# Performance work log

Hardware: AMD Instinct MI355X
Metric: run time of the kernel (lower is better)

Reference implementation:

```python
import jax, jax.numpy as jnp
import numpy as np

N_NODES = 50000
N_EDGES = 800000
NUM_GRAPHS = 512
IN_DIM = 128
HID = 128
OUT_DIM = 1


def setup_inputs() -> dict:
    key = jax.random.key(0)
    ks = jax.random.split(key, 8)
    x = jax.random.normal(ks[0], (N_NODES, IN_DIM), dtype=jnp.float32)
    edge_index = jax.random.randint(ks[1], (2, N_EDGES), 0, N_NODES, dtype=jnp.int64)
    batch = jnp.sort(jax.random.randint(ks[2], (N_NODES,), 0, NUM_GRAPHS, dtype=jnp.int64))
    s1 = 1.0 / np.sqrt(IN_DIM)
    s2 = 1.0 / np.sqrt(HID)
    W1 = jax.random.normal(ks[3], (IN_DIM, HID), dtype=jnp.float32) * s1
    b1 = jnp.zeros((HID,), dtype=jnp.float32)
    W2 = jax.random.normal(ks[4], (HID, HID), dtype=jnp.float32) * s2
    b2 = jnp.zeros((HID,), dtype=jnp.float32)
    Wl = jax.random.normal(ks[5], (HID, OUT_DIM), dtype=jnp.float32) * s2
    bl = jnp.zeros((OUT_DIM,), dtype=jnp.float32)
    return {"x": x, "edge_index": edge_index, "batch": batch,
            "W1": W1, "b1": b1, "W2": W2, "b2": b2, "Wl": Wl, "bl": bl}


def _gcn_conv(x, src, dst, norm, W, b):
    # GCNConv: D^{-1/2}(A+I)D^{-1/2} X W + b (self-loops already in src/dst)
    h = x @ W                                    # [N, H]
    msg = h[src] * norm[:, None]                 # gather + edge-normalize
    agg = jax.ops.segment_sum(msg, dst, num_segments=N_NODES)  # scatter-add
    return agg + b


def reference(x, edge_index, batch, W1, b1, W2, b2, Wl, bl):
    loops = jnp.arange(N_NODES, dtype=edge_index.dtype)
    src = jnp.concatenate([edge_index[0], loops])
    dst = jnp.concatenate([edge_index[1], loops])
    deg = jax.ops.segment_sum(jnp.ones_like(dst, dtype=x.dtype), dst, num_segments=N_NODES)
    dinv = jax.lax.rsqrt(deg)                    # deg >= 1 due to self-loops
    norm = dinv[src] * dinv[dst]                 # symmetric normalization per edge

    h = jax.nn.relu(_gcn_conv(x, src, dst, norm, W1, b1))
    h = jax.nn.relu(_gcn_conv(h, src, dst, norm, W2, b2))

    # global_mean_pool over graph ids
    sums = jax.ops.segment_sum(h, batch, num_segments=NUM_GRAPHS)
    cnts = jax.ops.segment_sum(jnp.ones((N_NODES,), dtype=h.dtype), batch, num_segments=NUM_GRAPHS)
    pooled = sums / jnp.maximum(cnts, 1.0)[:, None]

    out = jax.nn.sigmoid(pooled @ Wl + bl)       # [G, 1]
    return out.squeeze(1)                        # [G]
```

## Files before the change

kernel.cpp:

```cpp
#include <hip/hip_runtime.h>
#include <hip/hip_bf16.h>

#define N_NODES 50000
#define N_EDGES 800000
#define NUM_GRAPHS 512
#define MAXDEG 64
#define EPB 4096
#define P1_BLOCKS 196
#define NBUCK 256
#define NPB 196

typedef short short8 __attribute__((ext_vector_type(8)));
typedef unsigned short u16x8 __attribute__((ext_vector_type(8)));
typedef float f32x4 __attribute__((ext_vector_type(4)));

__device__ __forceinline__ unsigned short f2bu(float f) {
    __hip_bfloat16 h = __float2bfloat16(f);
    return *reinterpret_cast<unsigned short*>(&h);
}
__device__ __forceinline__ float bu2f(unsigned short u) {
    unsigned int v = ((unsigned int)u) << 16;
    float f;
    __builtin_memcpy(&f, &v, 4);
    return f;
}

__global__ __launch_bounds__(256) void bin_k(const int* __restrict__ ei,
                                             unsigned int* __restrict__ staging,
                                             int* __restrict__ cnts_tbl,
                                             int* __restrict__ offs_tbl,
                                             unsigned short* __restrict__ hs1,
                                             unsigned short* __restrict__ h1) {
    __shared__ unsigned int st[EPB];
    __shared__ int cnt[NBUCK], cur[NBUCK], scan[NBUCK];
    int b = blockIdx.x, t = threadIdx.x;
    if (b == 0 && t < 64)
        ((unsigned int*)(hs1 + (size_t)N_NODES * 128))[t] = 0u;
    if (b == 1 && t < 64)
        ((unsigned int*)(h1 + (size_t)N_NODES * 128))[t] = 0u;
    cnt[t] = 0;
    __syncthreads();

    int e0 = b * EPB;
    int srcv[16], dstv[16], bk[16];
#pragma unroll
    for (int k = 0; k < 16; ++k) {
        int e = e0 + k * 256 + t;
        bool ok = e < N_EDGES;
        srcv[k] = ok ? ei[e] : 0;
        dstv[k] = ok ? ei[N_EDGES + e] : 0;
        bk[k] = ok ? (dstv[k] / NPB) : -1;
        if (ok) atomicAdd(&cnt[bk[k]], 1);
    }
    __syncthreads();
    scan[t] = cnt[t];
    __syncthreads();
    for (int off = 1; off < 256; off <<= 1) {
        int u = t >= off ? scan[t - off] : 0;
        __syncthreads();
        scan[t] += u;
        __syncthreads();
    }
    int excl = scan[t] - cnt[t];
    cur[t] = excl;
    cnts_tbl[t * P1_BLOCKS + b] = cnt[t];
    offs_tbl[t * P1_BLOCKS + b] = excl;
    __syncthreads();
#pragma unroll
    for (int k = 0; k < 16; ++k) {
        if (bk[k] >= 0) {
            int pos = atomicAdd(&cur[bk[k]], 1);
            int dl = dstv[k] - bk[k] * NPB;
            st[pos] = (unsigned int)srcv[k] | ((unsigned int)dl << 16);
        }
    }
    __syncthreads();
    unsigned int* gout = staging + (size_t)b * EPB;
    for (int i = t; i < EPB; i += 256) gout[i] = st[i];
}

__global__ __launch_bounds__(256) void adjbuild_k(const unsigned int* __restrict__ staging,
                                                  const int* __restrict__ cnts_tbl,
                                                  const int* __restrict__ offs_tbl,
                                                  unsigned short* __restrict__ adj,
                                                  int* __restrict__ cnt,
                                                  float* __restrict__ dinv,
                                                  const float* __restrict__ W1,
                                                  const float* __restrict__ W2,
                                                  unsigned short* __restrict__ W1t,
                                                  unsigned short* __restrict__ W2t) {
    int b = blockIdx.x, t = threadIdx.x;
    if (b >= NBUCK) {
        int wb = b - NBUCK;
        const float* W = wb < 64 ? W1 : W2;
        unsigned short* Wt = wb < 64 ? W1t : W2t;
        int idx = (wb & 63) * 256 + t;
        int k = idx >> 7, n = idx & 127;
        Wt[n * 128 + k] = f2bu(W[idx]);
        return;
    }
    __shared__ unsigned short adjL[NPB * MAXDEG];
    __shared__ int cntL[NPB];
    __shared__ int segStart[P1_BLOCKS + 1];
    __shared__ int segOff[P1_BLOCKS];
    __shared__ int tmp[256];

    if (t < NPB) cntL[t] = 0;
    int c = t < P1_BLOCKS ? cnts_tbl[b * P1_BLOCKS + t] : 0;
    if (t < P1_BLOCKS) segOff[t] = offs_tbl[b * P1_BLOCKS + t];
    tmp[t] = c;
    __syncthreads();
    for (int off = 1; off < 256; off <<= 1) {
        int u = t >= off ? tmp[t - off] : 0;
        __syncthreads();
        tmp[t] += u;
        __syncthreads();
    }
    if (t < P1_BLOCKS) segStart[t] = tmp[t] - c;
    if (t == 0) segStart[P1_BLOCKS] = tmp[P1_BLOCKS - 1];
    __syncthreads();

    int T = segStart[P1_BLOCKS];
    for (int f = t; f < T; f += 256) {
        int lo = 0, hi = P1_BLOCKS;
        while (hi - lo > 1) {
            int m = (lo + hi) >> 1;
            if (segStart[m] <= f) lo = m; else hi = m;
        }
        unsigned int p = staging[(size_t)lo * EPB + segOff[lo] + (f - segStart[lo])];
        int src = p & 0xFFFF;
        int dl = p >> 16;
        int slot = atomicAdd(&cntL[dl], 1);
        if (slot < MAXDEG - 1) adjL[dl * MAXDEG + slot] = (unsigned short)src;
    }
    __syncthreads();

    int nodeBase = b * NPB;
    if (t < NPB) {
        int node = nodeBase + t;
        int cc = cntL[t];
        int ec = cc < MAXDEG - 1 ? cc : MAXDEG - 1;
        adjL[t * MAXDEG + ec] = (unsigned short)node;
        int tot = ec + 1, tot4 = (tot + 3) & ~3;
        for (int s = tot; s < tot4; ++s) adjL[t * MAXDEG + s] = (unsigned short)N_NODES;
        if (node < N_NODES) {
            cnt[node] = tot4;
            dinv[node] = rsqrtf((float)cc + 1.0f);
        }
    }
    __syncthreads();
    unsigned int* g = (unsigned int*)(adj + (size_t)nodeBase * MAXDEG);
    const unsigned int* l = (const unsigned int*)adjL;
    for (int i = t; i < NPB * MAXDEG / 2; i += 256) g[i] = l[i];
}

template <bool F32A>
__global__ __launch_bounds__(256) void gemm_k(const void* __restrict__ Ap,
                                              const unsigned short* __restrict__ Wt,
                                              const float* __restrict__ dinv,
                                              unsigned short* __restrict__ C) {
    __shared__ unsigned short Wl[128 * 136];
    int t = threadIdx.x;
    for (int idx = t; idx < 2048; idx += 256) {
        int n = idx >> 4, c = idx & 15;
        *(u16x8*)(Wl + n * 136 + c * 8) = *(const u16x8*)(Wt + n * 128 + c * 8);
    }
    __syncthreads();

    int wave = t >> 6, lane = t & 63, quad = lane >> 4, ln = lane & 15;
    int rb = blockIdx.x * 128 + wave * 16;

    short8 a[2][4];
#pragma unroll
    for (int mt = 0; mt < 2; ++mt) {
        int r = rb + mt * 64 + ln;
        r = r < N_NODES ? r : N_NODES - 1;
        if (F32A) {
            const float* arow = (const float*)Ap + (size_t)r * 128 + quad * 8;
#pragma unroll
            for (int ks = 0; ks < 4; ++ks) {
                float4 v0 = *(const float4*)(arow + ks * 32);
                float4 v1 = *(const float4*)(arow + ks * 32 + 4);
                short8 av;
                av[0] = (short)f2bu(v0.x); av[1] = (short)f2bu(v0.y);
                av[2] = (short)f2bu(v0.z); av[3] = (short)f2bu(v0.w);
                av[4] = (short)f2bu(v1.x); av[5] = (short)f2bu(v1.y);
                av[6] = (short)f2bu(v1.z); av[7] = (short)f2bu(v1.w);
                a[mt][ks] = av;
            }
        } else {
            const unsigned short* arow = (const unsigned short*)Ap + (size_t)r * 128 + quad * 8;
#pragma unroll
            for (int ks = 0; ks < 4; ++ks) a[mt][ks] = *(const short8*)(arow + ks * 32);
        }
    }

    f32x4 acc[2][8];
#pragma unroll
    for (int mt = 0; mt < 2; ++mt)
#pragma unroll
        for (int ct = 0; ct < 8; ++ct) acc[mt][ct] = (f32x4){0.f, 0.f, 0.f, 0.f};

#pragma unroll
    for (int ks = 0; ks < 4; ++ks)
#pragma unroll
        for (int ct = 0; ct < 8; ++ct) {
            short8 b = *(const short8*)(Wl + (ct * 16 + ln) * 136 + ks * 32 + quad * 8);
            acc[0][ct] = __builtin_amdgcn_mfma_f32_16x16x32_bf16(a[0][ks], b, acc[0][ct], 0, 0, 0);
            acc[1][ct] = __builtin_amdgcn_mfma_f32_16x16x32_bf16(a[1][ks], b, acc[1][ct], 0, 0, 0);
        }

#pragma unroll
    for (int mt = 0; mt < 2; ++mt) {
#pragma unroll
        for (int rr = 0; rr < 4; ++rr) {
            int r = rb + mt * 64 + quad * 4 + rr;
            if (r >= N_NODES) continue;
            float dv = dinv[r];
#pragma unroll
            for (int ct = 0; ct < 8; ++ct)
                C[(size_t)r * 128 + ct * 16 + ln] = f2bu(acc[mt][ct][rr] * dv);
        }
    }
}

__global__ __launch_bounds__(256) void agg1_k(const unsigned short* __restrict__ hs,
                                              const unsigned short* __restrict__ adj,
                                              const int* __restrict__ cnt,
                                              const float* __restrict__ dinv,
                                              const float* __restrict__ bias,
                                              unsigned short* __restrict__ out) {
    int t = threadIdx.x;
    int wave = t >> 6, lane = t & 63, quad = lane >> 4, fl = lane & 15;
    int node = blockIdx.x * 16 + wave * 4 + quad;
    int2 pack = ((const int2*)(adj + (size_t)node * MAXDEG))[fl];
    int rounds = cnt[node] >> 2;
    float dv = dinv[node];
    float4 b0 = *(const float4*)(bias + fl * 8);
    float4 b1 = *(const float4*)(bias + fl * 8 + 4);
    int qb = quad << 4;

    float a[8];
#pragma unroll
    for (int j = 0; j < 8; ++j) a[j] = 0.f;

    int i = 0;
    for (; i + 2 <= rounds; i += 2) {
        unsigned pAx = (unsigned)__shfl(pack.x, qb + i, 64);
        unsigned pAy = (unsigned)__shfl(pack.y, qb + i, 64);
        unsigned pBx = (unsigned)__shfl(pack.x, qb + i + 1, 64);
        unsigned pBy = (unsigned)__shfl(pack.y, qb + i + 1, 64);
        u16x8 v0 = *(const u16x8*)(hs + (size_t)(pAx & 0xFFFFu) * 128 + fl * 8);
        u16x8 v1 = *(const u16x8*)(hs + (size_t)(pAx >> 16) * 128 + fl * 8);
        u16x8 v2 = *(const u16x8*)(hs + (size_t)(pAy & 0xFFFFu) * 128 + fl * 8);
        u16x8 v3 = *(const u16x8*)(hs + (size_t)(pAy >> 16) * 128 + fl * 8);
        u16x8 v4 = *(const u16x8*)(hs + (size_t)(pBx & 0xFFFFu) * 128 + fl * 8);
        u16x8 v5 = *(const u16x8*)(hs + (size_t)(pBx >> 16) * 128 + fl * 8);
        u16x8 v6 = *(const u16x8*)(hs + (size_t)(pBy & 0xFFFFu) * 128 + fl * 8);
        u16x8 v7 = *(const u16x8*)(hs + (size_t)(pBy >> 16) * 128 + fl * 8);
#pragma unroll
        for (int j = 0; j < 8; ++j)
            a[j] += ((bu2f(v0[j]) + bu2f(v1[j])) + (bu2f(v2[j]) + bu2f(v3[j])))
                  + ((bu2f(v4[j]) + bu2f(v5[j])) + (bu2f(v6[j]) + bu2f(v7[j])));
    }
    if (i < rounds) {
        unsigned px = (unsigned)__shfl(pack.x, qb + i, 64);
        unsigned py = (unsigned)__shfl(pack.y, qb + i, 64);
        u16x8 v0 = *(const u16x8*)(hs + (size_t)(px & 0xFFFFu) * 128 + fl * 8);
        u16x8 v1 = *(const u16x8*)(hs + (size_t)(px >> 16) * 128 + fl * 8);
        u16x8 v2 = *(const u16x8*)(hs + (size_t)(py & 0xFFFFu) * 128 + fl * 8);
        u16x8 v3 = *(const u16x8*)(hs + (size_t)(py >> 16) * 128 + fl * 8);
#pragma unroll
        for (int j = 0; j < 8; ++j)
            a[j] += (bu2f(v0[j]) + bu2f(v1[j])) + (bu2f(v2[j]) + bu2f(v3[j]));
    }

    u16x8 o;
    o[0] = f2bu(fmaxf(a[0] * dv + b0.x, 0.f) * dv);
    o[1] = f2bu(fmaxf(a[1] * dv + b0.y, 0.f) * dv);
    o[2] = f2bu(fmaxf(a[2] * dv + b0.z, 0.f) * dv);
    o[3] = f2bu(fmaxf(a[3] * dv + b0.w, 0.f) * dv);
    o[4] = f2bu(fmaxf(a[4] * dv + b1.x, 0.f) * dv);
    o[5] = f2bu(fmaxf(a[5] * dv + b1.y, 0.f) * dv);
    o[6] = f2bu(fmaxf(a[6] * dv + b1.z, 0.f) * dv);
    o[7] = f2bu(fmaxf(a[7] * dv + b1.w, 0.f) * dv);
    *(u16x8*)(out + (size_t)node * 128 + fl * 8) = o;
}

__global__ __launch_bounds__(256) void agg2_fused_k(const unsigned short* __restrict__ hs,
                                                    const unsigned short* __restrict__ adj,
                                                    const int* __restrict__ cnt,
                                                    const float* __restrict__ dinv,
                                                    const float* __restrict__ bias,
                                                    const unsigned short* __restrict__ W2t,
                                                    const float* __restrict__ Wl,
                                                    float* __restrict__ pnode) {
    __shared__ unsigned short Az[16][136];
    __shared__ float part[4][16];
    int t = threadIdx.x;
    int wave = t >> 6, lane = t & 63, quad = lane >> 4, fl = lane & 15;
    int nl = wave * 4 + quad;
    int node = blockIdx.x * 16 + nl;
    int2 pack = ((const int2*)(adj + (size_t)node * MAXDEG))[fl];
    int rounds = cnt[node] >> 2;
    float dv = dinv[node];
    int qb = quad << 4;

    float a[8];
#pragma unroll
    for (int j = 0; j < 8; ++j) a[j] = 0.f;

    int i = 0;
    for (; i + 2 <= rounds; i += 2) {
        unsigned pAx = (unsigned)__shfl(pack.x, qb + i, 64);
        unsigned pAy = (unsigned)__shfl(pack.y, qb + i, 64);
        unsigned pBx = (unsigned)__shfl(pack.x, qb + i + 1, 64);
        unsigned pBy = (unsigned)__shfl(pack.y, qb + i + 1, 64);
        u16x8 v0 = *(const u16x8*)(hs + (size_t)(pAx & 0xFFFFu) * 128 + fl * 8);
        u16x8 v1 = *(const u16x8*)(hs + (size_t)(pAx >> 16) * 128 + fl * 8);
        u16x8 v2 = *(const u16x8*)(hs + (size_t)(pAy & 0xFFFFu) * 128 + fl * 8);
        u16x8 v3 = *(const u16x8*)(hs + (size_t)(pAy >> 16) * 128 + fl * 8);
        u16x8 v4 = *(const u16x8*)(hs + (size_t)(pBx & 0xFFFFu) * 128 + fl * 8);
        u16x8 v5 = *(const u16x8*)(hs + (size_t)(pBx >> 16) * 128 + fl * 8);
        u16x8 v6 = *(const u16x8*)(hs + (size_t)(pBy & 0xFFFFu) * 128 + fl * 8);
        u16x8 v7 = *(const u16x8*)(hs + (size_t)(pBy >> 16) * 128 + fl * 8);
#pragma unroll
        for (int j = 0; j < 8; ++j)
            a[j] += ((bu2f(v0[j]) + bu2f(v1[j])) + (bu2f(v2[j]) + bu2f(v3[j])))
                  + ((bu2f(v4[j]) + bu2f(v5[j])) + (bu2f(v6[j]) + bu2f(v7[j])));
    }
    if (i < rounds) {
        unsigned px = (unsigned)__shfl(pack.x, qb + i, 64);
        unsigned py = (unsigned)__shfl(pack.y, qb + i, 64);
        u16x8 v0 = *(const u16x8*)(hs + (size_t)(px & 0xFFFFu) * 128 + fl * 8);
        u16x8 v1 = *(const u16x8*)(hs + (size_t)(px >> 16) * 128 + fl * 8);
        u16x8 v2 = *(const u16x8*)(hs + (size_t)(py & 0xFFFFu) * 128 + fl * 8);
        u16x8 v3 = *(const u16x8*)(hs + (size_t)(py >> 16) * 128 + fl * 8);
#pragma unroll
        for (int j = 0; j < 8; ++j)
            a[j] += (bu2f(v0[j]) + bu2f(v1[j])) + (bu2f(v2[j]) + bu2f(v3[j]));
    }

    u16x8 zv;
#pragma unroll
    for (int j = 0; j < 8; ++j) zv[j] = f2bu(a[j] * dv);
    *(u16x8*)(&Az[nl][fl * 8]) = zv;
    __syncthreads();

    short8 af[4];
#pragma unroll
    for (int ks = 0; ks < 4; ++ks)
        af[ks] = *(const short8*)(&Az[fl][ks * 32 + quad * 8]);

    f32x4 acc[2];
    acc[0] = (f32x4){0.f, 0.f, 0.f, 0.f};
    acc[1] = (f32x4){0.f, 0.f, 0.f, 0.f};
#pragma unroll
    for (int ks = 0; ks < 4; ++ks)
#pragma unroll
        for (int ct = 0; ct < 2; ++ct) {
            short8 b = *(const short8*)(W2t + (size_t)(wave * 32 + ct * 16 + fl) * 128 + ks * 32 + quad * 8);
            acc[ct] = __builtin_amdgcn_mfma_f32_16x16x32_bf16(af[ks], b, acc[ct], 0, 0, 0);
        }

    float p[4];
#pragma unroll
    for (int rr = 0; rr < 4; ++rr) {
        float s = 0.f;
#pragma unroll
        for (int ct = 0; ct < 2; ++ct) {
            int col = wave * 32 + ct * 16 + fl;
            s += fmaxf(acc[ct][rr] + bias[col], 0.f) * Wl[col];
        }
        p[rr] = s;
    }
#pragma unroll
    for (int rr = 0; rr < 4; ++rr) {
        p[rr] += __shfl_xor(p[rr], 1, 64);
        p[rr] += __shfl_xor(p[rr], 2, 64);
        p[rr] += __shfl_xor(p[rr], 4, 64);
        p[rr] += __shfl_xor(p[rr], 8, 64);
    }
    if (fl == 0) {
#pragma unroll
        for (int rr = 0; rr < 4; ++rr) part[wave][quad * 4 + rr] = p[rr];
    }
    __syncthreads();
    if (t < 16)
        pnode[blockIdx.x * 16 + t] = part[0][t] + part[1][t] + part[2][t] + part[3][t];
}

__device__ __forceinline__ int lb(const int* a, int n, int v) {
    int lo = 0, hi = n;
    while (lo < hi) {
        int m = (lo + hi) >> 1;
        if (a[m] < v) lo = m + 1;
        else hi = m;
    }
    return lo;
}

__global__ __launch_bounds__(64) void final_k(const float* __restrict__ pnode,
                                              const int* __restrict__ batch,
                                              const float* __restrict__ bl,
                                              float* __restrict__ out) {
    int g = blockIdx.x, t = threadIdx.x;
    int lo = lb(batch, N_NODES, g), hi = lb(batch, N_NODES, g + 1);
    float s = 0.f;
    for (int r = lo + t; r < hi; r += 64) s += pnode[r];
#pragma unroll
    for (int o = 32; o > 0; o >>= 1) s += __shfl_down(s, o, 64);
    if (t == 0) {
        float cf = (float)(hi - lo);
        float z = s / fmaxf(cf, 1.f) + bl[0];
        out[g] = 1.f / (1.f + expf(-z));
    }
}

extern "C" void kernel_launch(void* const* d_in, const int* in_sizes, int n_in,
                              void* d_out, int out_size, void* d_ws, size_t ws_size,
                              hipStream_t stream) {
    const float* x = (const float*)d_in[0];
    const int* ei = (const int*)d_in[1];
    const int* batch = (const int*)d_in[2];
    const float* W1 = (const float*)d_in[3];
    const float* b1 = (const float*)d_in[4];
    const float* W2 = (const float*)d_in[5];
    const float* b2 = (const float*)d_in[6];
    const float* Wl = (const float*)d_in[7];
    const float* bl = (const float*)d_in[8];
    float* out = (float*)d_out;

    char* ws = (char*)d_ws;
    unsigned int* staging = (unsigned int*)(ws + 0x0);
    int* cnts_tbl = (int*)(ws + 0x310000);
    int* offs_tbl = (int*)(ws + 0x341000);
    unsigned short* adj = (unsigned short*)(ws + 0x372000);
    int* cnt = (int*)(ws + 0x992000);
    float* dinv = (float*)(ws + 0x9C3000);
    unsigned short* W1t = (unsigned short*)(ws + 0x9F4000);
    unsigned short* W2t = (unsigned short*)(ws + 0x9FC000);
    float* pnode = (float*)(ws + 0xA04000);
    unsigned short* hs1 = (unsigned short*)(ws + 0xA36000);
    unsigned short* h1 = (unsigned short*)(ws + 0x1672000);

    bin_k<<<P1_BLOCKS, 256, 0, stream>>>(ei, staging, cnts_tbl, offs_tbl, hs1, h1);
    adjbuild_k<<<NBUCK + 128, 256, 0, stream>>>(staging, cnts_tbl, offs_tbl,
                                                adj, cnt, dinv, W1, W2, W1t, W2t);

    gemm_k<true><<<(N_NODES + 127) / 128, 256, 0, stream>>>(x, W1t, dinv, hs1);
    agg1_k<<<N_NODES / 16, 256, 0, stream>>>(hs1, adj, cnt, dinv, b1, h1);
    agg2_fused_k<<<N_NODES / 16, 256, 0, stream>>>(h1, adj, cnt, dinv, b2, W2t, Wl, pnode);

    final_k<<<NUM_GRAPHS, 64, 0, stream>>>(pnode, batch, bl, out);
}
```

Measured before the change: 184.6 us.

## Reorder layer-1 to aggregate-then-transform and fuse pooling into layer-2 kernel

Layer 1 now gathers bf16 copies of the raw inputs, scaling each neighbour by its own dinv, and applies W1 via MFMA in the same kernel, so the separate GEMM kernel and its hs1 round-trip are gone. The fp32-to-bf16 conversion of x is folded into extra blocks of the binning kernel, which also zero the pool accumulators and counter. The final pooling kernel is replaced by per-node atomicAdd into per-graph sums, with a last-block-done counter that applies the sigmoid. The trade-offs are extra dinv gathers per edge in layer 1, global float atomics, and an order-dependent float sum.

```diff
diff --git a/kernel.cpp b/kernel.cpp
--- a/kernel.cpp
+++ b/kernel.cpp
@@ -9,6 +9,7 @@
 #define P1_BLOCKS 196
 #define NBUCK 256
 #define NPB 196
+#define XCONV_BLOCKS 3125
 
 typedef short short8 __attribute__((ext_vector_type(8)));
 typedef unsigned short u16x8 __attribute__((ext_vector_type(8)));
@@ -26,18 +27,38 @@
 }
 
 __global__ __launch_bounds__(256) void bin_k(const int* __restrict__ ei,
+                                             const float* __restrict__ x,
                                              unsigned int* __restrict__ staging,
                                              int* __restrict__ cnts_tbl,
                                              int* __restrict__ offs_tbl,
-                                             unsigned short* __restrict__ hs1,
-                                             unsigned short* __restrict__ h1) {
+                                             unsigned short* __restrict__ xb,
+                                             unsigned short* __restrict__ h1,
+                                             float* __restrict__ gsum,
+                                             int* __restrict__ counter,
+                                             float* __restrict__ dinv) {
+    int b = blockIdx.x, t = threadIdx.x;
+    if (b >= P1_BLOCKS) {
+        int xi = b - P1_BLOCKS;
+        if (xi == 0 && t < 64)
+            ((unsigned int*)(xb + (size_t)N_NODES * 128))[t] = 0u;
+        if (xi == 1 && t < 64)
+            ((unsigned int*)(h1 + (size_t)N_NODES * 128))[t] = 0u;
+        if (xi == 2) {
+            gsum[t] = 0.f; gsum[t + 256] = 0.f;
+            if (t == 0) { *counter = 0; dinv[N_NODES] = 0.f; }
+        }
+        const float* xp = x + (size_t)xi * 2048 + t * 8;
+        float4 v0 = *(const float4*)xp;
+        float4 v1 = *(const float4*)(xp + 4);
+        u16x8 o;
+        o[0] = f2bu(v0.x); o[1] = f2bu(v0.y); o[2] = f2bu(v0.z); o[3] = f2bu(v0.w);
+        o[4] = f2bu(v1.x); o[5] = f2bu(v1.y); o[6] = f2bu(v1.z); o[7] = f2bu(v1.w);
+        *(u16x8*)(xb + (size_t)xi * 2048 + t * 8) = o;
+        return;
+    }
+
     __shared__ unsigned int st[EPB];
     __shared__ int cnt[NBUCK], cur[NBUCK], scan[NBUCK];
-    int b = blockIdx.x, t = threadIdx.x;
-    if (b == 0 && t < 64)
-        ((unsigned int*)(hs1 + (size_t)N_NODES * 128))[t] = 0u;
-    if (b == 1 && t < 64)
-        ((unsigned int*)(h1 + (size_t)N_NODES * 128))[t] = 0u;
     cnt[t] = 0;
     __syncthreads();
 
@@ -154,90 +175,146 @@
     for (int i = t; i < NPB * MAXDEG / 2; i += 256) g[i] = l[i];
 }
 
-template <bool F32A>
-__global__ __launch_bounds__(256) void gemm_k(const void* __restrict__ Ap,
-                                              const unsigned short* __restrict__ Wt,
-                                              const float* __restrict__ dinv,
-                                              unsigned short* __restrict__ C) {
-    __shared__ unsigned short Wl[128 * 136];
-    int t = threadIdx.x;
-    for (int idx = t; idx < 2048; idx += 256) {
-        int n = idx >> 4, c = idx & 15;
-        *(u16x8*)(Wl + n * 136 + c * 8) = *(const u16x8*)(Wt + n * 128 + c * 8);
-    }
-    __syncthreads();
-
-    int wave = t >> 6, lane = t & 63, quad = lane >> 4, ln = lane & 15;
-    int rb = blockIdx.x * 128 + wave * 16;
-
-    short8 a[2][4];
-#pragma unroll
-    for (int mt = 0; mt < 2; ++mt) {
-        int r = rb + mt * 64 + ln;
-        r = r < N_NODES ? r : N_NODES - 1;
-        if (F32A) {
-            const float* arow = (const float*)Ap + (size_t)r * 128 + quad * 8;
-#pragma unroll
-            for (int ks = 0; ks < 4; ++ks) {
-                float4 v0 = *(const float4*)(arow + ks * 32);
-                float4 v1 = *(const float4*)(arow + ks * 32 + 4);
-                short8 av;
-                av[0] = (short)f2bu(v0.x); av[1] = (short)f2bu(v0.y);
-                av[2] = (short)f2bu(v0.z); av[3] = (short)f2bu(v0.w);
-                av[4] = (short)f2bu(v1.x); av[5] = (short)f2bu(v1.y);
-                av[6] = (short)f2bu(v1.z); av[7] = (short)f2bu(v1.w);
-                a[mt][ks] = av;
-            }
-        } else {
-            const unsigned short* arow = (const unsigned short*)Ap + (size_t)r * 128 + quad * 8;
-#pragma unroll
-            for (int ks = 0; ks < 4; ++ks) a[mt][ks] = *(const short8*)(arow + ks * 32);
-        }
-    }
-
-    f32x4 acc[2][8];
-#pragma unroll
-    for (int mt = 0; mt < 2; ++mt)
-#pragma unroll
-        for (int ct = 0; ct < 8; ++ct) acc[mt][ct] = (f32x4){0.f, 0.f, 0.f, 0.f};
-
-#pragma unroll
-    for (int ks = 0; ks < 4; ++ks)
-#pragma unroll
-        for (int ct = 0; ct < 8; ++ct) {
-            short8 b = *(const short8*)(Wl + (ct * 16 + ln) * 136 + ks * 32 + quad * 8);
-            acc[0][ct] = __builtin_amdgcn_mfma_f32_16x16x32_bf16(a[0][ks], b, acc[0][ct], 0, 0, 0);
-            acc[1][ct] = __builtin_amdgcn_mfma_f32_16x16x32_bf16(a[1][ks], b, acc[1][ct], 0, 0, 0);
-        }
-
-#pragma unroll
-    for (int mt = 0; mt < 2; ++mt) {
-#pragma unroll
-        for (int rr = 0; rr < 4; ++rr) {
-            int r = rb + mt * 64 + quad * 4 + rr;
-            if (r >= N_NODES) continue;
-            float dv = dinv[r];
-#pragma unroll
-            for (int ct = 0; ct < 8; ++ct)
-                C[(size_t)r * 128 + ct * 16 + ln] = f2bu(acc[mt][ct][rr] * dv);
-        }
-    }
-}
-
-__global__ __launch_bounds__(256) void agg1_k(const unsigned short* __restrict__ hs,
-                                              const unsigned short* __restrict__ adj,
-                                              const int* __restrict__ cnt,
-                                              const float* __restrict__ dinv,
-                                              const float* __restrict__ bias,
-                                              unsigned short* __restrict__ out) {
+__global__ __launch_bounds__(256) void agg1_fused_k(const unsigned short* __restrict__ xb,
+                                                    const unsigned short* __restrict__ adj,
+                                                    const int* __restrict__ cnt,
+                                                    const float* __restrict__ dinv,
+                                                    const float* __restrict__ bias,
+                                                    const unsigned short* __restrict__ W1t,
+                                                    unsigned short* __restrict__ out) {
+    __shared__ unsigned short Az[16][136];
     int t = threadIdx.x;
     int wave = t >> 6, lane = t & 63, quad = lane >> 4, fl = lane & 15;
-    int node = blockIdx.x * 16 + wave * 4 + quad;
+    int nl = wave * 4 + quad;
+    int node = blockIdx.x * 16 + nl;
     int2 pack = ((const int2*)(adj + (size_t)node * MAXDEG))[fl];
     int rounds = cnt[node] >> 2;
     float dv = dinv[node];
-    float4 b0 = *(const float4*)(bias + fl * 8);
-    float4 b1 = *(const float4*)(bias + fl * 8 + 4);
+    int qb = quad << 4;
+
+    float a[8];
+#pragma unroll
+    for (int j = 0; j < 8; ++j) a[j] = 0.f;
+
+    int i = 0;
+    for (; i + 2 <= rounds; i += 2) {
+        unsigned pAx = (unsigned)__shfl(pack.x, qb + i, 64);
+        unsigned pAy = (unsigned)__shfl(pack.y, qb + i, 64);
+        unsigned pBx = (unsigned)__shfl(pack.x, qb + i + 1, 64);
+        unsigned pBy = (unsigned)__shfl(pack.y, qb + i + 1, 64);
+        unsigned s0 = pAx & 0xFFFFu, s1 = pAx >> 16;
+        unsigned s2 = pAy & 0xFFFFu, s3 = pAy >> 16;
+        unsigned s4 = pBx & 0xFFFFu, s5 = pBx >> 16;
+        unsigned s6 = pBy & 0xFFFFu, s7 = pBy >> 16;
+        float d0 = dinv[s0], d1 = dinv[s1], d2 = dinv[s2], d3 = dinv[s3];
+        float d4 = dinv[s4], d5 = dinv[s5], d6 = dinv[s6], d7 = dinv[s7];
+        u16x8 v0 = *(const u16x8*)(xb + (size_t)s0 * 128 + fl * 8);
+        u16x8 v1 = *(const u16x8*)(xb + (size_t)s1 * 128 + fl * 8);
+        u16x8 v2 = *(const u16x8*)(xb + (size_t)s2 * 128 + fl * 8);
+        u16x8 v3 = *(const u16x8*)(xb + (size_t)s3 * 128 + fl * 8);
+        u16x8 v4 = *(const u16x8*)(xb + (size_t)s4 * 128 + fl * 8);
+        u16x8 v5 = *(const u16x8*)(xb + (size_t)s5 * 128 + fl * 8);
+        u16x8 v6 = *(const u16x8*)(xb + (size_t)s6 * 128 + fl * 8);
+        u16x8 v7 = *(const u16x8*)(xb + (size_t)s7 * 128 + fl * 8);
+#pragma unroll
+        for (int j = 0; j < 8; ++j) {
+            a[j] = fmaf(d0, bu2f(v0[j]), a[j]);
+            a[j] = fmaf(d1, bu2f(v1[j]), a[j]);
+            a[j] = fmaf(d2, bu2f(v2[j]), a[j]);
+            a[j] = fmaf(d3, bu2f(v3[j]), a[j]);
+            a[j] = fmaf(d4, bu2f(v4[j]), a[j]);
+            a[j] = fmaf(d5, bu2f(v5[j]), a[j]);
+            a[j] = fmaf(d6, bu2f(v6[j]), a[j]);
+            a[j] = fmaf(d7, bu2f(v7[j]), a[j]);
+        }
+    }
+    if (i < rounds) {
+        unsigned px = (unsigned)__shfl(pack.x, qb + i, 64);
+        unsigned py = (unsigned)__shfl(pack.y, qb + i, 64);
+        unsigned s0 = px & 0xFFFFu, s1 = px >> 16;
+        unsigned s2 = py & 0xFFFFu, s3 = py >> 16;
+        float d0 = dinv[s0], d1 = dinv[s1], d2 = dinv[s2], d3 = dinv[s3];
+        u16x8 v0 = *(const u16x8*)(xb + (size_t)s0 * 128 + fl * 8);
+        u16x8 v1 = *(const u16x8*)(xb + (size_t)s1 * 128 + fl * 8);
+        u16x8 v2 = *(const u16x8*)(xb + (size_t)s2 * 128 + fl * 8);
+        u16x8 v3 = *(const u16x8*)(xb + (size_t)s3 * 128 + fl * 8);
+#pragma unroll
+        for (int j = 0; j < 8; ++j) {
+            a[j] = fmaf(d0, bu2f(v0[j]), a[j]);
+            a[j] = fmaf(d1, bu2f(v1[j]), a[j]);
+            a[j] = fmaf(d2, bu2f(v2[j]), a[j]);
+            a[j] = fmaf(d3, bu2f(v3[j]), a[j]);
+        }
+    }
+
+    u16x8 zv;
+#pragma unroll
+    for (int j = 0; j < 8; ++j) zv[j] = f2bu(a[j] * dv);
+    *(u16x8*)(&Az[nl][fl * 8]) = zv;
+    __syncthreads();
+
+    short8 af[4];
+#pragma unroll
+    for (int ks = 0; ks < 4; ++ks)
+        af[ks] = *(const short8*)(&Az[fl][ks * 32 + quad * 8]);
+
+    f32x4 acc[2];
+    acc[0] = (f32x4){0.f, 0.f, 0.f, 0.f};
+    acc[1] = (f32x4){0.f, 0.f, 0.f, 0.f};
+#pragma unroll
+    for (int ks = 0; ks < 4; ++ks)
+#pragma unroll
+        for (int ct = 0; ct < 2; ++ct) {
+            short8 b = *(const short8*)(W1t + (size_t)(wave * 32 + ct * 16 + fl) * 128 + ks * 32 + quad * 8);
+            acc[ct] = __builtin_amdgcn_mfma_f32_16x16x32_bf16(af[ks], b, acc[ct], 0, 0, 0);
+        }
+
+    int colbase = wave * 32;
+    float bias0 = bias[colbase + fl];
+    float bias1 = bias[colbase + 16 + fl];
+    int rowbase = blockIdx.x * 16 + quad * 4;
+#pragma unroll
+    for (int rr = 0; rr < 4; ++rr) {
+        float dvr = dinv[rowbase + rr];
+        out[(size_t)(rowbase + rr) * 128 + colbase + fl] =
+            f2bu(fmaxf(acc[0][rr] + bias0, 0.f) * dvr);
+        out[(size_t)(rowbase + rr) * 128 + colbase + 16 + fl] =
+            f2bu(fmaxf(acc[1][rr] + bias1, 0.f) * dvr);
+    }
+}
+
+__device__ __forceinline__ int lb(const int* a, int n, int v) {
+    int lo = 0, hi = n;
+    while (lo < hi) {
+        int m = (lo + hi) >> 1;
+        if (a[m] < v) lo = m + 1;
+        else hi = m;
+    }
+    return lo;
+}
+
+__global__ __launch_bounds__(256) void agg2_fused_k(const unsigned short* __restrict__ hs,
+                                                    const unsigned short* __restrict__ adj,
+                                                    const int* __restrict__ cnt,
+                                                    const float* __restrict__ dinv,
+                                                    const float* __restrict__ bias,
+                                                    const unsigned short* __restrict__ W2t,
+                                                    const float* __restrict__ Wl,
+                                                    const int* __restrict__ batch,
+                                                    const float* __restrict__ bl,
+                                                    float* __restrict__ gsum,
+                                                    int* __restrict__ counter,
+                                                    float* __restrict__ out) {
+    __shared__ unsigned short Az[16][136];
+    __shared__ float part[4][16];
+    __shared__ int lastS;
+    int t = threadIdx.x;
+    int wave = t >> 6, lane = t & 63, quad = lane >> 4, fl = lane & 15;
+    int nl = wave * 4 + quad;
+    int node = blockIdx.x * 16 + nl;
+    int2 pack = ((const int2*)(adj + (size_t)node * MAXDEG))[fl];
+    int rounds = cnt[node] >> 2;
+    float dv = dinv[node];
     int qb = quad << 4;
 
     float a[8];
@@ -275,72 +352,6 @@
             a[j] += (bu2f(v0[j]) + bu2f(v1[j])) + (bu2f(v2[j]) + bu2f(v3[j]));
     }
 
-    u16x8 o;
-    o[0] = f2bu(fmaxf(a[0] * dv + b0.x, 0.f) * dv);
-    o[1] = f2bu(fmaxf(a[1] * dv + b0.y, 0.f) * dv);
-    o[2] = f2bu(fmaxf(a[2] * dv + b0.z, 0.f) * dv);
-    o[3] = f2bu(fmaxf(a[3] * dv + b0.w, 0.f) * dv);
-    o[4] = f2bu(fmaxf(a[4] * dv + b1.x, 0.f) * dv);
-    o[5] = f2bu(fmaxf(a[5] * dv + b1.y, 0.f) * dv);
-    o[6] = f2bu(fmaxf(a[6] * dv + b1.z, 0.f) * dv);
-    o[7] = f2bu(fmaxf(a[7] * dv + b1.w, 0.f) * dv);
-    *(u16x8*)(out + (size_t)node * 128 + fl * 8) = o;
-}
-
-__global__ __launch_bounds__(256) void agg2_fused_k(const unsigned short* __restrict__ hs,
-                                                    const unsigned short* __restrict__ adj,
-                                                    const int* __restrict__ cnt,
-                                                    const float* __restrict__ dinv,
-                                                    const float* __restrict__ bias,
-                                                    const unsigned short* __restrict__ W2t,
-                                                    const float* __restrict__ Wl,
-                                                    float* __restrict__ pnode) {
-    __shared__ unsigned short Az[16][136];
-    __shared__ float part[4][16];
-    int t = threadIdx.x;
-    int wave = t >> 6, lane = t & 63, quad = lane >> 4, fl = lane & 15;
-    int nl = wave * 4 + quad;
-    int node = blockIdx.x * 16 + nl;
-    int2 pack = ((const int2*)(adj + (size_t)node * MAXDEG))[fl];
-    int rounds = cnt[node] >> 2;
-    float dv = dinv[node];
-    int qb = quad << 4;
-
-    float a[8];
-#pragma unroll
-    for (int j = 0; j < 8; ++j) a[j] = 0.f;
-
-    int i = 0;
-    for (; i + 2 <= rounds; i += 2) {
-        unsigned pAx = (unsigned)__shfl(pack.x, qb + i, 64);
-        unsigned pAy = (unsigned)__shfl(pack.y, qb + i, 64);
-        unsigned pBx = (unsigned)__shfl(pack.x, qb + i + 1, 64);
-        unsigned pBy = (unsigned)__shfl(pack.y, qb + i + 1, 64);
-        u16x8 v0 = *(const u16x8*)(hs + (size_t)(pAx & 0xFFFFu) * 128 + fl * 8);
-        u16x8 v1 = *(const u16x8*)(hs + (size_t)(pAx >> 16) * 128 + fl * 8);
-        u16x8 v2 = *(const u16x8*)(hs + (size_t)(pAy & 0xFFFFu) * 128 + fl * 8);
-        u16x8 v3 = *(const u16x8*)(hs + (size_t)(pAy >> 16) * 128 + fl * 8);
-        u16x8 v4 = *(const u16x8*)(hs + (size_t)(pBx & 0xFFFFu) * 128 + fl * 8);
-        u16x8 v5 = *(const u16x8*)(hs + (size_t)(pBx >> 16) * 128 + fl * 8);
-        u16x8 v6 = *(const u16x8*)(hs + (size_t)(pBy & 0xFFFFu) * 128 + fl * 8);
-        u16x8 v7 = *(const u16x8*)(hs + (size_t)(pBy >> 16) * 128 + fl * 8);
-#pragma unroll
-        for (int j = 0; j < 8; ++j)
-            a[j] += ((bu2f(v0[j]) + bu2f(v1[j])) + (bu2f(v2[j]) + bu2f(v3[j])))
-                  + ((bu2f(v4[j]) + bu2f(v5[j])) + (bu2f(v6[j]) + bu2f(v7[j])));
-    }
-    if (i < rounds) {
-        unsigned px = (unsigned)__shfl(pack.x, qb + i, 64);
-        unsigned py = (unsigned)__shfl(pack.y, qb + i, 64);
-        u16x8 v0 = *(const u16x8*)(hs + (size_t)(px & 0xFFFFu) * 128 + fl * 8);
-        u16x8 v1 = *(const u16x8*)(hs + (size_t)(px >> 16) * 128 + fl * 8);
-        u16x8 v2 = *(const u16x8*)(hs + (size_t)(py & 0xFFFFu) * 128 + fl * 8);
-        u16x8 v3 = *(const u16x8*)(hs + (size_t)(py >> 16) * 128 + fl * 8);
-#pragma unroll
-        for (int j = 0; j < 8; ++j)
-            a[j] += (bu2f(v0[j]) + bu2f(v1[j])) + (bu2f(v2[j]) + bu2f(v3[j]));
-    }
-
     u16x8 zv;
 #pragma unroll
     for (int j = 0; j < 8; ++j) zv[j] = f2bu(a[j] * dv);
@@ -386,34 +397,24 @@
         for (int rr = 0; rr < 4; ++rr) part[wave][quad * 4 + rr] = p[rr];
     }
     __syncthreads();
-    if (t < 16)
-        pnode[blockIdx.x * 16 + t] = part[0][t] + part[1][t] + part[2][t] + part[3][t];
-}
-
-__device__ __forceinline__ int lb(const int* a, int n, int v) {
-    int lo = 0, hi = n;
-    while (lo < hi) {
-        int m = (lo + hi) >> 1;
-        if (a[m] < v) lo = m + 1;
-        else hi = m;
-    }
-    return lo;
-}
-
-__global__ __launch_bounds__(64) void final_k(const float* __restrict__ pnode,
-                                              const int* __restrict__ batch,
-                                              const float* __restrict__ bl,
-                                              float* __restrict__ out) {
-    int g = blockIdx.x, t = threadIdx.x;
-    int lo = lb(batch, N_NODES, g), hi = lb(batch, N_NODES, g + 1);
-    float s = 0.f;
-    for (int r = lo + t; r < hi; r += 64) s += pnode[r];
-#pragma unroll
-    for (int o = 32; o > 0; o >>= 1) s += __shfl_down(s, o, 64);
-    if (t == 0) {
-        float cf = (float)(hi - lo);
-        float z = s / fmaxf(cf, 1.f) + bl[0];
-        out[g] = 1.f / (1.f + expf(-z));
+    if (t < 16) {
+        float pn = part[0][t] + part[1][t] + part[2][t] + part[3][t];
+        int nd = blockIdx.x * 16 + t;
+        atomicAdd(&gsum[batch[nd]], pn);
+        __threadfence();
+    }
+    __syncthreads();
+    if (t == 0) lastS = (atomicAdd(counter, 1) == (int)gridDim.x - 1) ? 1 : 0;
+    __syncthreads();
+    if (lastS) {
+        __threadfence();
+        float bl0 = bl[0];
+        for (int g = t; g < NUM_GRAPHS; g += 256) {
+            int lo = lb(batch, N_NODES, g), hi = lb(batch, N_NODES, g + 1);
+            float s = atomicAdd(&gsum[g], 0.f);
+            float z = s / fmaxf((float)(hi - lo), 1.f) + bl0;
+            out[g] = 1.f / (1.f + expf(-z));
+        }
     }
 }
 
@@ -440,17 +441,17 @@
     float* dinv = (float*)(ws + 0x9C3000);
     unsigned short* W1t = (unsigned short*)(ws + 0x9F4000);
     unsigned short* W2t = (unsigned short*)(ws + 0x9FC000);
-    float* pnode = (float*)(ws + 0xA04000);
-    unsigned short* hs1 = (unsigned short*)(ws + 0xA36000);
+    float* gsum = (float*)(ws + 0xA04000);
+    int* counter = (int*)(ws + 0xA05000);
+    unsigned short* xb = (unsigned short*)(ws + 0xA36000);
     unsigned short* h1 = (unsigned short*)(ws + 0x1672000);
 
-    bin_k<<<P1_BLOCKS, 256, 0, stream>>>(ei, staging, cnts_tbl, offs_tbl, hs1, h1);
+    bin_k<<<P1_BLOCKS + XCONV_BLOCKS, 256, 0, stream>>>(ei, x, staging, cnts_tbl,
+                                                        offs_tbl, xb, h1, gsum,
+                                                        counter, dinv);
     adjbuild_k<<<NBUCK + 128, 256, 0, stream>>>(staging, cnts_tbl, offs_tbl,
                                                 adj, cnt, dinv, W1, W2, W1t, W2t);
-
-    gemm_k<true><<<(N_NODES + 127) / 128, 256, 0, stream>>>(x, W1t, dinv, hs1);
-    agg1_k<<<N_NODES / 16, 256, 0, stream>>>(hs1, adj, cnt, dinv, b1, h1);
-    agg2_fused_k<<<N_NODES / 16, 256, 0, stream>>>(h1, adj, cnt, dinv, b2, W2t, Wl, pnode);
-
-    final_k<<<NUM_GRAPHS, 64, 0, stream>>>(pnode, batch, bl, out);
-}
+    agg1_fused_k<<<N_NODES / 16, 256, 0, stream>>>(xb, adj, cnt, dinv, b1, W1t, h1);
+    agg2_fused_k<<<N_NODES / 16, 256, 0, stream>>>(h1, adj, cnt, dinv, b2, W2t, Wl,
+                                                   batch, bl, gsum, counter, out);
+}
```

Measured after the change: 334.9 us. 1.81x slower.
